# Optimization experiments

Hardware: AMD Instinct MI355X
Metric: run time of the kernel (lower is better)

## Reference

```python
import jax, jax.numpy as jnp
import numpy as np

N_EMBD = 768
N_HEAD = 12
HEAD_DIM = N_EMBD // N_HEAD


def setup_inputs() -> dict:
    key = jax.random.key(0)
    k1, k2, k3 = jax.random.split(key, 3)
    x = jax.random.normal(k1, (2, 2048, N_EMBD), dtype=jnp.float32)
    # Dense kernels (no bias), scaled like Glorot-ish init
    w_qkv = jax.random.normal(k2, (N_EMBD, 3 * N_EMBD), dtype=jnp.float32) * (1.0 / np.sqrt(N_EMBD))
    w_proj = jax.random.normal(k3, (N_EMBD, N_EMBD), dtype=jnp.float32) * (1.0 / np.sqrt(N_EMBD))
    return {"x": x, "w_qkv": w_qkv, "w_proj": w_proj}


def reference(x, w_qkv, w_proj):
    b, t, _ = x.shape
    qkv = x @ w_qkv                                  # [b, t, 3*n_embd]
    q, k, v = jnp.split(qkv, 3, axis=-1)
    def split_heads(z):
        return z.reshape(b, t, N_HEAD, HEAD_DIM).transpose(0, 2, 1, 3)  # [b, h, t, d]
    q, k, v = split_heads(q), split_heads(k), split_heads(v)
    scale = jnp.float32(HEAD_DIM) ** -0.5
    att = jnp.einsum('bhqd,bhkd->bhqk', q, k) * scale  # [b, h, t, t]
    # lower-triangular causal mask, additive -1e9 on masked (future) positions
    mask = jnp.tril(jnp.ones((t, t), dtype=jnp.float32))
    att = att + (1.0 - mask)[None, None, :, :] * jnp.float32(-1e9)
    att = jax.nn.softmax(att, axis=-1)
    out = jnp.einsum('bhqk,bhkd->bhqd', att, v)      # [b, h, t, d]
    out = out.transpose(0, 2, 1, 3).reshape(b, t, N_EMBD)
    return out @ w_proj
```

## Files before the change

kernel.cpp:

```cpp
#include <hip/hip_runtime.h>

#define T_SEQ   2048
#define EMBD    768
#define N_HEAD  12
#define HDIM    64
#define BATCH   2

typedef float f32x4 __attribute__((ext_vector_type(4)));
typedef short bf16x8 __attribute__((ext_vector_type(8)));
typedef unsigned short u16;
typedef u16 u16x4 __attribute__((ext_vector_type(4)));

#define MFMA_BF16(a, b, c) __builtin_amdgcn_mfma_f32_16x16x32_bf16((a), (b), (c), 0, 0, 0)

__device__ __forceinline__ u16 f2bf(float f) {
    union { float f; unsigned u; } v; v.f = f;
    unsigned r = v.u + 0x7fffu + ((v.u >> 16) & 1u);
    return (u16)(r >> 16);
}

__global__ __launch_bounds__(256) void convert_bf16(
    const float* __restrict__ x, u16* __restrict__ y, int n)
{
    const int i = (blockIdx.x * 256 + threadIdx.x) * 8;
    if (i >= n) return;
    const float4 f0 = *(const float4*)&x[i];
    const float4 f1 = *(const float4*)&x[i + 4];
    bf16x8 r;
    r[0] = (short)f2bf(f0.x); r[1] = (short)f2bf(f0.y);
    r[2] = (short)f2bf(f0.z); r[3] = (short)f2bf(f0.w);
    r[4] = (short)f2bf(f1.x); r[5] = (short)f2bf(f1.y);
    r[6] = (short)f2bf(f1.z); r[7] = (short)f2bf(f1.w);
    *(bf16x8*)&y[i] = r;
}

__global__ __launch_bounds__(256) void convert_wT(
    const float* __restrict__ W, u16* __restrict__ Wt, int N)
{
    __shared__ float tile[32][33];
    const int c  = threadIdx.x & 31;
    const int r8 = threadIdx.x >> 5;
    const int n0 = blockIdx.x * 32;
    const int k0 = blockIdx.y * 32;
#pragma unroll
    for (int rr = r8; rr < 32; rr += 8)
        tile[rr][c] = W[(size_t)(k0 + rr) * N + n0 + c];
    __syncthreads();
#pragma unroll
    for (int rr = r8; rr < 32; rr += 8)
        Wt[(size_t)(n0 + rr) * 768 + k0 + c] = f2bf(tile[c][rr]);
}

template <int NCOLS, int SCATTER>
__global__ __launch_bounds__(256) void mfma_gemm(
    const u16* __restrict__ A, const u16* __restrict__ Bt,
    float* __restrict__ C, u16* __restrict__ Qo, u16* __restrict__ Ko,
    u16* __restrict__ Vo)
{
    __shared__ u16 As[128 * 40];
    __shared__ u16 Bs[128 * 40];
    const int tid  = threadIdx.x;
    const int lane = tid & 63, wave = tid >> 6;
    const int l15  = lane & 15, quad = lane >> 4;
    const int wy   = wave >> 1, wx = wave & 1;
    const int row0 = blockIdx.y * 128, col0 = blockIdx.x * 128;
    const int sr   = tid >> 2;
    const int sk   = (tid & 3) * 8;

    f32x4 acc[4][4];
#pragma unroll
    for (int i = 0; i < 4; ++i)
#pragma unroll
        for (int j = 0; j < 4; ++j) acc[i][j] = (f32x4){0.f, 0.f, 0.f, 0.f};

    for (int k0 = 0; k0 < 768; k0 += 32) {
        const bf16x8 a0 = *(const bf16x8*)&A[(size_t)(row0 + sr) * 768 + k0 + sk];
        const bf16x8 a1 = *(const bf16x8*)&A[(size_t)(row0 + sr + 64) * 768 + k0 + sk];
        const bf16x8 b0 = *(const bf16x8*)&Bt[(size_t)(col0 + sr) * 768 + k0 + sk];
        const bf16x8 b1 = *(const bf16x8*)&Bt[(size_t)(col0 + sr + 64) * 768 + k0 + sk];
        __syncthreads();
        *(bf16x8*)&As[sr * 40 + sk]        = a0;
        *(bf16x8*)&As[(sr + 64) * 40 + sk] = a1;
        *(bf16x8*)&Bs[sr * 40 + sk]        = b0;
        *(bf16x8*)&Bs[(sr + 64) * 40 + sk] = b1;
        __syncthreads();
        bf16x8 af[4], bfr[4];
#pragma unroll
        for (int mt = 0; mt < 4; ++mt)
            af[mt] = *(const bf16x8*)&As[(wy * 64 + mt * 16 + l15) * 40 + quad * 8];
#pragma unroll
        for (int nt = 0; nt < 4; ++nt)
            bfr[nt] = *(const bf16x8*)&Bs[(wx * 64 + nt * 16 + l15) * 40 + quad * 8];
#pragma unroll
        for (int mt = 0; mt < 4; ++mt)
#pragma unroll
            for (int nt = 0; nt < 4; ++nt)
                acc[mt][nt] = MFMA_BF16(af[mt], bfr[nt], acc[mt][nt]);
    }

#pragma unroll
    for (int mt = 0; mt < 4; ++mt) {
#pragma unroll
        for (int nt = 0; nt < 4; ++nt) {
            const int col = col0 + wx * 64 + nt * 16 + l15;
            if (SCATTER) {
                const int which = col / 768;
                const int hh = (col - which * 768) >> 6;
                const int dd = col & 63;
                if (which == 2) {
                    const int row = row0 + wy * 64 + mt * 16 + quad * 4;
                    const int bb = row >> 11, t0 = row & 2047;
                    u16x4 pk;
#pragma unroll
                    for (int r = 0; r < 4; ++r) pk[r] = f2bf(acc[mt][nt][r]);
                    *(u16x4*)&Vo[((size_t)(bb * N_HEAD + hh) * HDIM + dd) * T_SEQ + t0] = pk;
                } else {
                    u16* dst = (which == 0) ? Qo : Ko;
                    const size_t hb = (size_t)hh * T_SEQ * HDIM + dd;
#pragma unroll
                    for (int r = 0; r < 4; ++r) {
                        const int row = row0 + wy * 64 + mt * 16 + quad * 4 + r;
                        const int bb = row >> 11, tt = row & 2047;
                        dst[(size_t)bb * N_HEAD * T_SEQ * HDIM + hb + (size_t)tt * HDIM] =
                            f2bf(acc[mt][nt][r]);
                    }
                }
            } else {
#pragma unroll
                for (int r = 0; r < 4; ++r) {
                    const int row = row0 + wy * 64 + mt * 16 + quad * 4 + r;
                    C[(size_t)row * NCOLS + col] = acc[mt][nt][r];
                }
            }
        }
    }
}

__global__ __launch_bounds__(256, 3) void attn_mfma(
    const u16* __restrict__ Q, const u16* __restrict__ K,
    const u16* __restrict__ Vt, u16* __restrict__ Aout)
{
    __shared__ u16  Ps[4][32 * 72];
    __shared__ float Comb[2][40 * 64];

    const int tid  = threadIdx.x;
    const int lane = tid & 63, wave = tid >> 6;
    const int l15  = lane & 15, quad = lane >> 4;

    const int f    = blockIdx.x;
    const int slot = f >> 3;
    const int p    = slot & 31;
    const int bh   = (f & 7) * 3 + (slot >> 5);
    const int b    = bh / N_HEAD, h = bh - b * N_HEAD;

    const int j      = (wave < 2) ? p : (63 - p);
    const int parity = wave & 1;
    const int qb     = j * 32;
    const int nk     = (j >> 1) + 1;
    const size_t base = (size_t)bh * T_SEQ * HDIM;

    bf16x8 qf[2][2];
#pragma unroll
    for (int jq = 0; jq < 2; ++jq)
#pragma unroll
        for (int ks = 0; ks < 2; ++ks)
            qf[jq][ks] = *(const bf16x8*)&Q[base + (size_t)(qb + jq * 16 + l15) * HDIM +
                                            ks * 32 + quad * 8];

    f32x4 o[2][4], l_acc[2];
#pragma unroll
    for (int jq = 0; jq < 2; ++jq) {
        l_acc[jq] = (f32x4){0.f, 0.f, 0.f, 0.f};
#pragma unroll
        for (int nt = 0; nt < 4; ++nt) o[jq][nt] = (f32x4){0.f, 0.f, 0.f, 0.f};
    }

    bf16x8 onesf;
#pragma unroll
    for (int jj = 0; jj < 8; ++jj) onesf[jj] = (short)0x3F80;

    u16* myPs = &Ps[wave][0];

    for (int kt = parity; kt < nk; kt += 2) {
        const int k0 = kt * 64;

        bf16x8 vf[4][2];
#pragma unroll
        for (int nt = 0; nt < 4; ++nt)
#pragma unroll
            for (int ks = 0; ks < 2; ++ks)
                vf[nt][ks] = *(const bf16x8*)&Vt[base + (size_t)(nt * 16 + l15) * T_SEQ +
                                                 k0 + ks * 32 + quad * 8];

        f32x4 s[4][2];
#pragma unroll
        for (int i = 0; i < 4; ++i)
#pragma unroll
            for (int jq = 0; jq < 2; ++jq) s[i][jq] = (f32x4){0.f, 0.f, 0.f, 0.f};
#pragma unroll
        for (int ks = 0; ks < 2; ++ks) {
            bf16x8 kf[4];
#pragma unroll
            for (int i = 0; i < 4; ++i)
                kf[i] = *(const bf16x8*)&K[base + (size_t)(k0 + i * 16 + l15) * HDIM +
                                           ks * 32 + quad * 8];
#pragma unroll
            for (int i = 0; i < 4; ++i)
#pragma unroll
                for (int jq = 0; jq < 2; ++jq)
                    s[i][jq] = MFMA_BF16(kf[i], qf[jq][ks], s[i][jq]);
        }

        const bool need_mask = (k0 + 63 > qb);
#pragma unroll
        for (int i = 0; i < 4; ++i)
#pragma unroll
            for (int jq = 0; jq < 2; ++jq) {
                u16x4 pk;
#pragma unroll
                for (int r = 0; r < 4; ++r) {
                    float v = s[i][jq][r] * 0.125f;
                    if (need_mask) {
                        const int key = k0 + i * 16 + quad * 4 + r;
                        const int q   = qb + jq * 16 + l15;
                        if (key > q) v = -1e30f;
                    }
                    pk[r] = f2bf(__expf(v));
                }
                *(u16x4*)&myPs[(jq * 16 + l15) * 72 + i * 16 + quad * 4] = pk;
            }

#pragma unroll
        for (int ks = 0; ks < 2; ++ks) {
            bf16x8 pa[2];
#pragma unroll
            for (int jq = 0; jq < 2; ++jq)
                pa[jq] = *(const bf16x8*)&myPs[(jq * 16 + l15) * 72 + ks * 32 + quad * 8];
#pragma unroll
            for (int jq = 0; jq < 2; ++jq) {
#pragma unroll
                for (int nt = 0; nt < 4; ++nt)
                    o[jq][nt] = MFMA_BF16(pa[jq], vf[nt][ks], o[jq][nt]);
                l_acc[jq] = MFMA_BF16(pa[jq], onesf, l_acc[jq]);
            }
        }
    }

    if (parity == 1) {
        float* cb = &Comb[wave >> 1][0];
#pragma unroll
        for (int jq = 0; jq < 2; ++jq) {
#pragma unroll
            for (int nt = 0; nt < 4; ++nt)
#pragma unroll
                for (int r = 0; r < 4; ++r)
                    cb[(jq * 16 + nt * 4 + r) * 64 + lane] = o[jq][nt][r];
#pragma unroll
            for (int r = 0; r < 4; ++r)
                cb[(32 + jq * 4 + r) * 64 + lane] = l_acc[jq][r];
        }
    }
    __syncthreads();
    if (parity == 0) {
        const float* cb = &Comb[wave >> 1][0];
#pragma unroll
        for (int jq = 0; jq < 2; ++jq) {
#pragma unroll
            for (int nt = 0; nt < 4; ++nt)
#pragma unroll
                for (int r = 0; r < 4; ++r)
                    o[jq][nt][r] += cb[(jq * 16 + nt * 4 + r) * 64 + lane];
#pragma unroll
            for (int r = 0; r < 4; ++r)
                l_acc[jq][r] += cb[(32 + jq * 4 + r) * 64 + lane];
        }
#pragma unroll
        for (int jq = 0; jq < 2; ++jq) {
            f32x4 inv;
#pragma unroll
            for (int r = 0; r < 4; ++r) inv[r] = 1.0f / l_acc[jq][r];
#pragma unroll
            for (int nt = 0; nt < 4; ++nt) {
                const int d = nt * 16 + l15;
#pragma unroll
                for (int r = 0; r < 4; ++r) {
                    const int q = qb + jq * 16 + quad * 4 + r;
                    Aout[(size_t)(b * T_SEQ + q) * EMBD + h * HDIM + d] =
                        f2bf(o[jq][nt][r] * inv[r]);
                }
            }
        }
    }
}

extern "C" void kernel_launch(void* const* d_in, const int* in_sizes, int n_in,
                              void* d_out, int out_size, void* d_ws, size_t ws_size,
                              hipStream_t stream)
{
    (void)in_sizes; (void)n_in; (void)out_size; (void)ws_size;
    const float* x      = (const float*)d_in[0];
    const float* w_qkv  = (const float*)d_in[1];
    const float* w_proj = (const float*)d_in[2];
    float* out = (float*)d_out;

    u16* ws = (u16*)d_ws;
    const size_t NX  = (size_t)BATCH * T_SEQ * EMBD;
    const size_t NWQ = (size_t)EMBD * 3 * EMBD;
    const size_t NWP = (size_t)EMBD * EMBD;
    const size_t SZ  = (size_t)BATCH * N_HEAD * T_SEQ * HDIM;
    u16* xb     = ws;
    u16* wqkvT  = xb + NX;
    u16* wprojT = wqkvT + NWQ;
    u16* Qb     = wprojT + NWP;
    u16* Kb     = Qb + SZ;
    u16* Vtb    = Kb + SZ;
    u16* Ab     = Vtb + SZ;

    dim3 blk(256);
    convert_bf16<<<dim3((int)(NX / 2048)), blk, 0, stream>>>(x, xb, (int)NX);
    convert_wT<<<dim3(3 * EMBD / 32, EMBD / 32), blk, 0, stream>>>(w_qkv, wqkvT, 3 * EMBD);
    convert_wT<<<dim3(EMBD / 32, EMBD / 32), blk, 0, stream>>>(w_proj, wprojT, EMBD);

    mfma_gemm<3 * EMBD, 1><<<dim3(3 * EMBD / 128, BATCH * T_SEQ / 128), blk, 0, stream>>>(
        xb, wqkvT, nullptr, Qb, Kb, Vtb);

    attn_mfma<<<dim3(32 * N_HEAD * BATCH), blk, 0, stream>>>(Qb, Kb, Vtb, Ab);

    mfma_gemm<EMBD, 0><<<dim3(EMBD / 128, BATCH * T_SEQ / 128), blk, 0, stream>>>(
        Ab, wprojT, out, nullptr, nullptr, nullptr);
}
```

Baseline: 191.0 us.

## Restructure attention work split, use direct-to-LDS GEMM loads, fold softmax scale into Q

The GEMM now stages tiles with global_load_lds into an XOR-swizzled, unpadded LDS layout instead of going through registers, and sets a 2-blocks occupancy hint. The Q projection is pre-multiplied by scale*log2(e) so attention uses exp2f without a per-element multiply, and bf16 packing uses a perm truncation instead of round-to-nearest. Attention now gives each block one 32-row query tile, splits its key tiles across 4 waves, and reduces them through shared memory that is reused from the P buffers. The grid doubles in size and the occupancy hint rises to 4; the cost is a longer cross-wave reduction and truncation rounding of P.

Result: slower. 219.2 us (+14.8%).

```diff
diff --git a/kernel.cpp b/kernel.cpp
--- a/kernel.cpp
+++ b/kernel.cpp
@@ -9,6 +9,7 @@
 typedef float f32x4 __attribute__((ext_vector_type(4)));
 typedef short bf16x8 __attribute__((ext_vector_type(8)));
 typedef unsigned short u16;
+typedef unsigned int u32;
 typedef u16 u16x4 __attribute__((ext_vector_type(4)));
 
 #define MFMA_BF16(a, b, c) __builtin_amdgcn_mfma_f32_16x16x32_bf16((a), (b), (c), 0, 0, 0)
@@ -17,6 +18,18 @@
     union { float f; unsigned u; } v; v.f = f;
     unsigned r = v.u + 0x7fffu + ((v.u >> 16) & 1u);
     return (u16)(r >> 16);
+}
+
+__device__ __forceinline__ u32 pack2(float hi, float lo) {
+    union { float f; u32 u; } a, b;
+    a.f = hi; b.f = lo;
+    return __builtin_amdgcn_perm(a.u, b.u, 0x07060302u);
+}
+
+__device__ __forceinline__ void gload_lds16(const u16* g, u16* l) {
+    __builtin_amdgcn_global_load_lds(
+        (const __attribute__((address_space(1))) u32*)g,
+        (__attribute__((address_space(3))) u32*)l, 16, 0, 0);
 }
 
 __global__ __launch_bounds__(256) void convert_bf16(
@@ -52,20 +65,32 @@
 }
 
 template <int NCOLS, int SCATTER>
-__global__ __launch_bounds__(256) void mfma_gemm(
+__global__ __launch_bounds__(256, 2) void mfma_gemm(
     const u16* __restrict__ A, const u16* __restrict__ Bt,
     float* __restrict__ C, u16* __restrict__ Qo, u16* __restrict__ Ko,
     u16* __restrict__ Vo)
 {
-    __shared__ u16 As[128 * 40];
-    __shared__ u16 Bs[128 * 40];
+    __shared__ u16 As[128 * 32];
+    __shared__ u16 Bs[128 * 32];
     const int tid  = threadIdx.x;
     const int lane = tid & 63, wave = tid >> 6;
     const int l15  = lane & 15, quad = lane >> 4;
     const int wy   = wave >> 1, wx = wave & 1;
     const int row0 = blockIdx.y * 128, col0 = blockIdx.x * 128;
-    const int sr   = tid >> 2;
-    const int sk   = (tid & 3) * 8;
+
+    const int sr = lane >> 2;
+    const int sc = lane & 3;
+    const int sg = sc ^ (sr & 3) ^ (sr >> 2);
+    const u16* gA0 = &A [(size_t)(row0 + wave * 16 + sr) * 768 + sg * 8];
+    const u16* gA1 = &A [(size_t)(row0 + 64 + wave * 16 + sr) * 768 + sg * 8];
+    const u16* gB0 = &Bt[(size_t)(col0 + wave * 16 + sr) * 768 + sg * 8];
+    const u16* gB1 = &Bt[(size_t)(col0 + 64 + wave * 16 + sr) * 768 + sg * 8];
+    u16* lA0 = &As[wave * 512];
+    u16* lA1 = &As[2048 + wave * 512];
+    u16* lB0 = &Bs[wave * 512];
+    u16* lB1 = &Bs[2048 + wave * 512];
+
+    const int sw = (l15 & 3) ^ (l15 >> 2);
 
     f32x4 acc[4][4];
 #pragma unroll
@@ -74,23 +99,19 @@
         for (int j = 0; j < 4; ++j) acc[i][j] = (f32x4){0.f, 0.f, 0.f, 0.f};
 
     for (int k0 = 0; k0 < 768; k0 += 32) {
-        const bf16x8 a0 = *(const bf16x8*)&A[(size_t)(row0 + sr) * 768 + k0 + sk];
-        const bf16x8 a1 = *(const bf16x8*)&A[(size_t)(row0 + sr + 64) * 768 + k0 + sk];
-        const bf16x8 b0 = *(const bf16x8*)&Bt[(size_t)(col0 + sr) * 768 + k0 + sk];
-        const bf16x8 b1 = *(const bf16x8*)&Bt[(size_t)(col0 + sr + 64) * 768 + k0 + sk];
         __syncthreads();
-        *(bf16x8*)&As[sr * 40 + sk]        = a0;
-        *(bf16x8*)&As[(sr + 64) * 40 + sk] = a1;
-        *(bf16x8*)&Bs[sr * 40 + sk]        = b0;
-        *(bf16x8*)&Bs[(sr + 64) * 40 + sk] = b1;
+        gload_lds16(gA0 + k0, lA0);
+        gload_lds16(gA1 + k0, lA1);
+        gload_lds16(gB0 + k0, lB0);
+        gload_lds16(gB1 + k0, lB1);
         __syncthreads();
         bf16x8 af[4], bfr[4];
 #pragma unroll
         for (int mt = 0; mt < 4; ++mt)
-            af[mt] = *(const bf16x8*)&As[(wy * 64 + mt * 16 + l15) * 40 + quad * 8];
+            af[mt] = *(const bf16x8*)&As[(wy * 64 + mt * 16 + l15) * 32 + ((quad ^ sw) * 8)];
 #pragma unroll
         for (int nt = 0; nt < 4; ++nt)
-            bfr[nt] = *(const bf16x8*)&Bs[(wx * 64 + nt * 16 + l15) * 40 + quad * 8];
+            bfr[nt] = *(const bf16x8*)&Bs[(wx * 64 + nt * 16 + l15) * 32 + ((quad ^ sw) * 8)];
 #pragma unroll
         for (int mt = 0; mt < 4; ++mt)
 #pragma unroll
@@ -98,6 +119,7 @@
                 acc[mt][nt] = MFMA_BF16(af[mt], bfr[nt], acc[mt][nt]);
     }
 
+    const float qscale = 0.18033688f;
 #pragma unroll
     for (int mt = 0; mt < 4; ++mt) {
 #pragma unroll
@@ -116,13 +138,14 @@
                     *(u16x4*)&Vo[((size_t)(bb * N_HEAD + hh) * HDIM + dd) * T_SEQ + t0] = pk;
                 } else {
                     u16* dst = (which == 0) ? Qo : Ko;
+                    const float sc2 = (which == 0) ? qscale : 1.0f;
                     const size_t hb = (size_t)hh * T_SEQ * HDIM + dd;
 #pragma unroll
                     for (int r = 0; r < 4; ++r) {
                         const int row = row0 + wy * 64 + mt * 16 + quad * 4 + r;
                         const int bb = row >> 11, tt = row & 2047;
                         dst[(size_t)bb * N_HEAD * T_SEQ * HDIM + hb + (size_t)tt * HDIM] =
-                            f2bf(acc[mt][nt][r]);
+                            f2bf(acc[mt][nt][r] * sc2);
                     }
                 }
             } else {
@@ -136,27 +159,24 @@
     }
 }
 
-__global__ __launch_bounds__(256, 3) void attn_mfma(
+__global__ __launch_bounds__(256, 4) void attn_mfma(
     const u16* __restrict__ Q, const u16* __restrict__ K,
     const u16* __restrict__ Vt, u16* __restrict__ Aout)
 {
-    __shared__ u16  Ps[4][32 * 72];
-    __shared__ float Comb[2][40 * 64];
+    __shared__ float Comb[5120];
+    u16* PsAll = (u16*)Comb;
 
     const int tid  = threadIdx.x;
     const int lane = tid & 63, wave = tid >> 6;
     const int l15  = lane & 15, quad = lane >> 4;
 
-    const int f    = blockIdx.x;
-    const int slot = f >> 3;
-    const int p    = slot & 31;
-    const int bh   = (f & 7) * 3 + (slot >> 5);
-    const int b    = bh / N_HEAD, h = bh - b * N_HEAD;
-
-    const int j      = (wave < 2) ? p : (63 - p);
-    const int parity = wave & 1;
-    const int qb     = j * 32;
-    const int nk     = (j >> 1) + 1;
+    const int f  = blockIdx.x;
+    const int g  = f >> 3;
+    const int bh = (f & 7) * 3 + (g >> 6);
+    const int j  = 63 - (g & 63);
+    const int b  = bh / N_HEAD, h = bh - b * N_HEAD;
+    const int qb = j * 32;
+    const int nk = (j >> 1) + 1;
     const size_t base = (size_t)bh * T_SEQ * HDIM;
 
     bf16x8 qf[2][2];
@@ -177,11 +197,11 @@
 
     bf16x8 onesf;
 #pragma unroll
-    for (int jj = 0; jj < 8; ++jj) onesf[jj] = (short)0x3F80;
-
-    u16* myPs = &Ps[wave][0];
-
-    for (int kt = parity; kt < nk; kt += 2) {
+    for (int u = 0; u < 8; ++u) onesf[u] = (short)0x3F80;
+
+    u16* myPs = PsAll + wave * 2304;
+
+    for (int kt = wave; kt < nk; kt += 4) {
         const int k0 = kt * 64;
 
         bf16x8 vf[4][2];
@@ -216,18 +236,22 @@
         for (int i = 0; i < 4; ++i)
 #pragma unroll
             for (int jq = 0; jq < 2; ++jq) {
-                u16x4 pk;
-#pragma unroll
-                for (int r = 0; r < 4; ++r) {
-                    float v = s[i][jq][r] * 0.125f;
-                    if (need_mask) {
+                float pv[4];
+                if (need_mask) {
+                    const int q = qb + jq * 16 + l15;
+#pragma unroll
+                    for (int r = 0; r < 4; ++r) {
                         const int key = k0 + i * 16 + quad * 4 + r;
-                        const int q   = qb + jq * 16 + l15;
-                        if (key > q) v = -1e30f;
+                        pv[r] = exp2f((key > q) ? -1e30f : s[i][jq][r]);
                     }
-                    pk[r] = f2bf(__expf(v));
+                } else {
+#pragma unroll
+                    for (int r = 0; r < 4; ++r) pv[r] = exp2f(s[i][jq][r]);
                 }
-                *(u16x4*)&myPs[(jq * 16 + l15) * 72 + i * 16 + quad * 4] = pk;
+                uint2 w;
+                w.x = pack2(pv[1], pv[0]);
+                w.y = pack2(pv[3], pv[2]);
+                *(uint2*)&myPs[(jq * 16 + l15) * 72 + i * 16 + quad * 4] = w;
             }
 
 #pragma unroll
@@ -246,33 +270,63 @@
         }
     }
 
-    if (parity == 1) {
-        float* cb = &Comb[wave >> 1][0];
+    __syncthreads();
+    float* R0 = Comb;
+    float* R1 = Comb + 2560;
+    if (wave == 1 || wave == 3) {
+        float* R = (wave == 1) ? R0 : R1;
 #pragma unroll
         for (int jq = 0; jq < 2; ++jq) {
 #pragma unroll
             for (int nt = 0; nt < 4; ++nt)
 #pragma unroll
                 for (int r = 0; r < 4; ++r)
-                    cb[(jq * 16 + nt * 4 + r) * 64 + lane] = o[jq][nt][r];
+                    R[(jq * 16 + nt * 4 + r) * 64 + lane] = o[jq][nt][r];
 #pragma unroll
             for (int r = 0; r < 4; ++r)
-                cb[(32 + jq * 4 + r) * 64 + lane] = l_acc[jq][r];
+                R[(32 + jq * 4 + r) * 64 + lane] = l_acc[jq][r];
         }
     }
     __syncthreads();
-    if (parity == 0) {
-        const float* cb = &Comb[wave >> 1][0];
+    if (wave == 0 || wave == 2) {
+        float* R = (wave == 0) ? R0 : R1;
 #pragma unroll
         for (int jq = 0; jq < 2; ++jq) {
 #pragma unroll
             for (int nt = 0; nt < 4; ++nt)
 #pragma unroll
                 for (int r = 0; r < 4; ++r)
-                    o[jq][nt][r] += cb[(jq * 16 + nt * 4 + r) * 64 + lane];
+                    o[jq][nt][r] += R[(jq * 16 + nt * 4 + r) * 64 + lane];
 #pragma unroll
             for (int r = 0; r < 4; ++r)
-                l_acc[jq][r] += cb[(32 + jq * 4 + r) * 64 + lane];
+                l_acc[jq][r] += R[(32 + jq * 4 + r) * 64 + lane];
+        }
+        if (wave == 2) {
+#pragma unroll
+            for (int jq = 0; jq < 2; ++jq) {
+#pragma unroll
+                for (int nt = 0; nt < 4; ++nt)
+#pragma unroll
+                    for (int r = 0; r < 4; ++r)
+                        R1[(jq * 16 + nt * 4 + r) * 64 + lane] = o[jq][nt][r];
+#pragma unroll
+                for (int r = 0; r < 4; ++r)
+                    R1[(32 + jq * 4 + r) * 64 + lane] = l_acc[jq][r];
+            }
+        }
+    }
+    __syncthreads();
+    if (wave == 0) {
+#pragma unroll
+        for (int jq = 0; jq < 2; ++jq) {
+#pragma unroll
+            for (int nt = 0; nt < 4; ++nt)
+#pragma unroll
+                for (int r = 0; r < 4; ++r)
+                    o[jq][nt][r] += R1[(jq * 16 + nt * 4 + r) * 64 + lane];
+#pragma unroll
+            for (int r = 0; r < 4; ++r)
+                l_acc[jq][r] += R1[(32 + jq * 4 + r) * 64 + lane];
         }
 #pragma unroll
         for (int jq = 0; jq < 2; ++jq) {
@@ -324,7 +378,7 @@
     mfma_gemm<3 * EMBD, 1><<<dim3(3 * EMBD / 128, BATCH * T_SEQ / 128), blk, 0, stream>>>(
         xb, wqkvT, nullptr, Qb, Kb, Vtb);
 
-    attn_mfma<<<dim3(32 * N_HEAD * BATCH), blk, 0, stream>>>(Qb, Kb, Vtb, Ab);
+    attn_mfma<<<dim3(64 * N_HEAD * BATCH), blk, 0, stream>>>(Qb, Kb, Vtb, Ab);
 
     mfma_gemm<EMBD, 0><<<dim3(EMBD / 128, BATCH * T_SEQ / 128), blk, 0, stream>>>(
         Ab, wprojT, out, nullptr, nullptr, nullptr);
```
